# Optimization experiments

Measured on AMD Instinct MI355X. Metric: run time of the kernel, lower is better.

The kernel has to match this reference:

```python
import math
import jax, jax.numpy as jnp
import numpy as np

L, H, E, D = 12, 12, 768, 64   # stack_size, mh_size, embedding_dim, dim_w_matrices
B, S = 4, 512
EPS = 1e-5


def positional_enc(seq_len, model_dim):
    # faithful: power_ind = 10000 XOR int(2*i/dim)
    i = np.arange(model_dim)
    p = np.bitwise_xor(10000, (2 * i) // model_dim).astype(np.float32)
    pos = np.arange(seq_len, dtype=np.float32)[:, None]
    ang = pos / p[None, :]
    pe = np.where(i % 2 == 0, np.sin(ang), np.cos(ang)).astype(np.float32)
    return jnp.asarray(pe)


def layer_norm(x, g, b):
    mu = jnp.mean(x, axis=-1, keepdims=True)
    var = jnp.mean(jnp.square(x - mu), axis=-1, keepdims=True)
    return (x - mu) * jax.lax.rsqrt(var + EPS) * g + b


def encoder(x, wq, wo, g1, b1, fw, fb, g2, b2):
    # x: [B,S,E]; wq: [H,E,D]; wo: [E,H*D]; fw: [E,E] (torch Linear layout)
    bs = x.shape[0] * x.shape[1]
    nb = x.reshape(bs, E)                              # flatten batch (faithful)
    q = jnp.einsum('ne,hed->hnd', nb, wq)              # q == k == v (bug kept)
    scores = jax.nn.softmax(jnp.einsum('hnd,hmd->hnm', q, q) / math.sqrt(D), axis=-1)
    z = jnp.einsum('hnm,hmd->hnd', scores, q)          # [H,BS,D]
    zc = z.reshape(H * D, bs)                          # per-head view(D,-1) + cat
    mh = (wo @ zc).reshape(x.shape)                    # [B,S,E]
    l1 = layer_norm(x + mh, g1, b1)
    ffn = l1 @ fw.T + fb
    return layer_norm(l1 + ffn, g2, b2)


def setup_inputs() -> dict:
    key = jax.random.key(0)
    ks = jax.random.split(key, 8)

    def xavier(k, shape, fan_in, fan_out):
        lim = math.sqrt(6.0 / (fan_in + fan_out))
        return jax.random.uniform(k, shape, jnp.float32, -lim, lim)

    return {
        'tokens': jax.random.normal(ks[0], (B, S, E), jnp.float32),
        'wq':    xavier(ks[1], (L, H, E, D), E, D),
        'wo':    xavier(ks[2], (L, E, H * D), E, H * D),
        'ln1_g': jnp.ones((L, E), jnp.float32),
        'ln1_b': jnp.zeros((L, E), jnp.float32),
        'ffn_w': xavier(ks[3], (L, E, E), E, E),
        'ffn_b': jnp.zeros((L, E), jnp.float32),
        'ln2_g': jnp.ones((L, E), jnp.float32),
        'ln2_b': jnp.zeros((L, E), jnp.float32),
    }


def reference(tokens, wq, wo, ln1_g, ln1_b, ffn_w, ffn_b, ln2_g, ln2_b):
    pe = positional_enc(tokens.shape[1], tokens.shape[2])
    # faithful: layer 0 applied once on pe+tokens, then ALL layers (0 again) in loop
    x = encoder(pe + tokens, wq[0], wo[0], ln1_g[0], ln1_b[0],
                ffn_w[0], ffn_b[0], ln2_g[0], ln2_b[0])
    for l in range(L):
        x = encoder(x, wq[l], wo[l], ln1_g[l], ln1_b[l],
                    ffn_w[l], ffn_b[l], ln2_g[l], ln2_b[l])
    return x
```

## Files before the change

kernel.cpp:

```cpp
#include <hip/hip_runtime.h>
#include <hip/hip_bf16.h>


#define BS_TOK 2048
#define EMB 768
#define NH 12
#define HD 64
#define WQN (12 * NH * EMB * HD)

typedef __attribute__((ext_vector_type(8))) short bf16x8;
typedef __attribute__((ext_vector_type(4))) float f32x4;

__device__ __forceinline__ short f2bf(float f) {
  union { float f; unsigned u; } v;
  v.f = f;
  unsigned r = (v.u + 0x7FFF + ((v.u >> 16) & 1)) >> 16;
  return (short)(unsigned short)r;
}

#define MFMA16(a, b, c) __builtin_amdgcn_mfma_f32_16x16x32_bf16(a, b, c, 0, 0, 0)
#define SW64(r, k) ((r) * 64 + ((((k) >> 3) ^ ((r) & 7)) << 3) + ((k) & 7))

__global__ __launch_bounds__(256) void cvt_weights_kernel(const float* __restrict__ wo,
                                                          const float* __restrict__ fw,
                                                          short* __restrict__ wob,
                                                          short* __restrict__ fwb) {
  const float* src = blockIdx.y ? fw : wo;
  short* dst = blockIdx.y ? fwb : wob;
  int i = (blockIdx.x * 256 + threadIdx.x) * 8;
  float4 a = *(const float4*)(src + i);
  float4 b = *(const float4*)(src + i + 4);
  bf16x8 t;
  t[0] = f2bf(a.x); t[1] = f2bf(a.y); t[2] = f2bf(a.z); t[3] = f2bf(a.w);
  t[4] = f2bf(b.x); t[5] = f2bf(b.y); t[6] = f2bf(b.z); t[7] = f2bf(b.w);
  *(bf16x8*)(dst + i) = t;
}

__global__ __launch_bounds__(256) void wq_trans_kernel(const float* __restrict__ wq,
                                                       short* __restrict__ wqT) {
  __shared__ short T[64 * 64];
  const int et = blockIdx.x;
  const int lh = blockIdx.y;
  const int tid = threadIdx.x;
  const float* src = wq + ((size_t)lh * EMB + et * 64) * HD;
  {
    int r = tid >> 2, c16 = (tid & 3) << 4;
    const float* p = src + r * HD + c16;
    float4 x0 = *(const float4*)(p + 0);
    float4 x1 = *(const float4*)(p + 4);
    float4 x2 = *(const float4*)(p + 8);
    float4 x3 = *(const float4*)(p + 12);
    bf16x8 a, b;
    a[0] = f2bf(x0.x); a[1] = f2bf(x0.y); a[2] = f2bf(x0.z); a[3] = f2bf(x0.w);
    a[4] = f2bf(x1.x); a[5] = f2bf(x1.y); a[6] = f2bf(x1.z); a[7] = f2bf(x1.w);
    b[0] = f2bf(x2.x); b[1] = f2bf(x2.y); b[2] = f2bf(x2.z); b[3] = f2bf(x2.w);
    b[4] = f2bf(x3.x); b[5] = f2bf(x3.y); b[6] = f2bf(x3.z); b[7] = f2bf(x3.w);
    int g = c16 >> 3;
    *(bf16x8*)&T[r * 64 + ((g ^ (r & 7)) << 3)] = a;
    *(bf16x8*)&T[r * 64 + (((g + 1) ^ (r & 7)) << 3)] = b;
  }
  __syncthreads();
  {
    int d = tid >> 2, e16 = (tid & 3) << 4;
    bf16x8 t0, t1;
#pragma unroll
    for (int j = 0; j < 8; ++j) t0[j] = T[SW64(e16 + j, d)];
#pragma unroll
    for (int j = 0; j < 8; ++j) t1[j] = T[SW64(e16 + 8 + j, d)];
    short* q = wqT + ((size_t)lh * HD + d) * EMB + et * 64 + e16;
    *(bf16x8*)(q) = t0;
    *(bf16x8*)(q + 8) = t1;
  }
}

__global__ __launch_bounds__(256) void pe_add_kernel(const float* __restrict__ tok,
                                                     float* __restrict__ X,
                                                     short* __restrict__ Xb) {
  int idx = blockIdx.x * 256 + threadIdx.x;
  int e = idx % EMB;
  int t = idx / EMB;
  int s = t & 511;
  float p = (e < 384) ? 10000.0f : 10001.0f;
  float ang = (float)s / p;
  float pe = (e & 1) ? cosf(ang) : sinf(ang);
  float v = tok[idx] + pe;
  X[idx] = v;
  Xb[idx] = f2bf(v);
}

__device__ __forceinline__ void stage_direct_bf16(const short* __restrict__ src, int ld,
                                                  int row0, int k0, short* dst, int tid) {
  int r = tid >> 2, kb = (tid & 3) << 4;
  const short* p = src + (size_t)(row0 + r) * ld + k0 + kb;
  bf16x8 x0 = *(const bf16x8*)(p);
  bf16x8 x1 = *(const bf16x8*)(p + 8);
  int g = kb >> 3;
  *(bf16x8*)&dst[r * 64 + ((g ^ (r & 7)) << 3)] = x0;
  *(bf16x8*)&dst[r * 64 + (((g + 1) ^ (r & 7)) << 3)] = x1;
}

__device__ __forceinline__ void stage_direct128(const short* __restrict__ src, int ld,
                                                int row0, int k0, short* dst, int tid) {
  int r = tid >> 1, kb = (tid & 1) << 5;
  const short* p = src + (size_t)(row0 + r) * ld + k0 + kb;
  bf16x8 x0 = *(const bf16x8*)(p);
  bf16x8 x1 = *(const bf16x8*)(p + 8);
  bf16x8 x2 = *(const bf16x8*)(p + 16);
  bf16x8 x3 = *(const bf16x8*)(p + 24);
  int g = kb >> 3;
  *(bf16x8*)&dst[r * 64 + (((g + 0) ^ (r & 7)) << 3)] = x0;
  *(bf16x8*)&dst[r * 64 + (((g + 1) ^ (r & 7)) << 3)] = x1;
  *(bf16x8*)&dst[r * 64 + (((g + 2) ^ (r & 7)) << 3)] = x2;
  *(bf16x8*)&dst[r * 64 + (((g + 3) ^ (r & 7)) << 3)] = x3;
}

__device__ __forceinline__ void stage_trans_bf16(const short* __restrict__ src, int ld,
                                                 int k0, int col0, short* dst, int tid) {
  int kk = tid >> 2, nb = (tid & 3) << 4;
  const short* p = src + (size_t)(k0 + kk) * ld + col0 + nb;
  bf16x8 x0 = *(const bf16x8*)(p + 0);
  bf16x8 x1 = *(const bf16x8*)(p + 8);
#pragma unroll
  for (int j = 0; j < 8; ++j) dst[SW64(nb + j, kk)] = x0[j];
#pragma unroll
  for (int j = 0; j < 8; ++j) dst[SW64(nb + 8 + j, kk)] = x1[j];
}

#define GEMM_TILE_COMPUTE(As, Bs, acc)                                              \
  {                                                                                 \
    _Pragma("unroll") for (int s = 0; s < 2; ++s) {                                 \
      int ra = (w << 4) + l15;                                                      \
      bf16x8 af = *(const bf16x8*)&As[ra * 64 + ((((s << 2) + quad) ^ (ra & 7)) << 3)]; \
      _Pragma("unroll") for (int nt = 0; nt < 4; ++nt) {                            \
        int rb = (nt << 4) + l15;                                                   \
        bf16x8 bf = *(const bf16x8*)&Bs[rb * 64 + ((((s << 2) + quad) ^ (rb & 7)) << 3)]; \
        acc[nt] = MFMA16(af, bf, acc[nt]);                                          \
      }                                                                             \
    }                                                                               \
  }

#define GEMM_TILE_COMPUTE2(As, Bs, acc)                                             \
  {                                                                                 \
    _Pragma("unroll") for (int s = 0; s < 2; ++s) {                                 \
      bf16x8 af[2];                                                                 \
      _Pragma("unroll") for (int u = 0; u < 2; ++u) {                               \
        int ra = (w << 5) + (u << 4) + l15;                                         \
        af[u] = *(const bf16x8*)&As[ra * 64 + ((((s << 2) + quad) ^ (ra & 7)) << 3)]; \
      }                                                                             \
      _Pragma("unroll") for (int nt = 0; nt < 4; ++nt) {                            \
        int rb = (nt << 4) + l15;                                                   \
        bf16x8 bf = *(const bf16x8*)&Bs[rb * 64 + ((((s << 2) + quad) ^ (rb & 7)) << 3)]; \
        acc[0][nt] = MFMA16(af[0], bf, acc[0][nt]);                                 \
        acc[1][nt] = MFMA16(af[1], bf, acc[1][nt]);                                 \
      }                                                                             \
    }                                                                               \
  }

__global__ __launch_bounds__(256) void gemm_q_kernel(const short* __restrict__ Xb,
                                                     const short* __restrict__ WqT,
                                                     short* __restrict__ Qo,
                                                     short* __restrict__ Qt) {
  __shared__ short As[64 * 64];
  __shared__ short Bs[64 * 64];
  const int m0 = blockIdx.x * 64;
  const int h = blockIdx.y;
  const int tid = threadIdx.x;
  const int w = tid >> 6, lane = tid & 63, l15 = lane & 15, quad = lane >> 4;
  const short* wqh = WqT + (size_t)h * (HD * EMB);
  f32x4 acc[4] = {(f32x4){0, 0, 0, 0}, (f32x4){0, 0, 0, 0},
                  (f32x4){0, 0, 0, 0}, (f32x4){0, 0, 0, 0}};
  for (int k0 = 0; k0 < EMB; k0 += 64) {
    stage_direct_bf16(Xb, EMB, m0, k0, As, tid);
    stage_direct_bf16(wqh, EMB, 0, k0, Bs, tid);
    __syncthreads();
    GEMM_TILE_COMPUTE(As, Bs, acc);
    __syncthreads();
  }
  short* qo = Qo + (size_t)h * (BS_TOK * HD);
#pragma unroll
  for (int nt = 0; nt < 4; ++nt)
#pragma unroll
    for (int r = 0; r < 4; ++r) {
      short v = f2bf(acc[nt][r]);
      int tokr = (w << 4) + (quad << 2) + r;
      int d = (nt << 4) + l15;
      qo[(size_t)(m0 + tokr) * HD + d] = v;
      As[SW64(tokr, d)] = v;
    }
  __syncthreads();
  {
    int d = tid >> 2, tok0 = (tid & 3) << 4;
    bf16x8 t0, t1;
#pragma unroll
    for (int j = 0; j < 8; ++j) t0[j] = As[SW64(tok0 + j, d)];
#pragma unroll
    for (int j = 0; j < 8; ++j) t1[j] = As[SW64(tok0 + 8 + j, d)];
    short* qt = Qt + (size_t)h * (HD * BS_TOK) + (size_t)d * BS_TOK + m0 + tok0;
    *(bf16x8*)(qt) = t0;
    *(bf16x8*)(qt + 8) = t1;
  }
}

__global__ __launch_bounds__(256) void attn_mfma_kernel(const short* __restrict__ Q,
                                                        const short* __restrict__ Qt,
                                                        float* __restrict__ Opart,
                                                        float* __restrict__ Lpart) {
  __shared__ short Ks[64 * 64];
  __shared__ short Vt[64 * 64];
  __shared__ short Pw[4 * 16 * 64];
  const int h = blockIdx.y;
  const int q0 = blockIdx.x * 64;
  const int kt0 = blockIdx.z * 16;
  const int tid = threadIdx.x;
  const int lane = tid & 63;
  const int wv = tid >> 6;
  const int l15 = lane & 15;
  const int quad = lane >> 4;
  const short* Qh = Q + (size_t)h * (BS_TOK * HD);
  const short* Qth = Qt + (size_t)h * (HD * BS_TOK);
  short* myP = Pw + wv * 16 * 64;

  bf16x8 qf[2];
  {
    const short* qp = Qh + (size_t)(q0 + wv * 16 + l15) * HD + quad * 8;
    qf[0] = *(const bf16x8*)(qp);
    qf[1] = *(const bf16x8*)(qp + 32);
  }

  f32x4 o[4];
  float lp[4] = {0.f, 0.f, 0.f, 0.f};
#pragma unroll
  for (int r = 0; r < 4; ++r) o[r] = (f32x4){0.f, 0.f, 0.f, 0.f};

  bf16x8 kreg[2], vreg[2];
#pragma unroll
  for (int i = 0; i < 2; ++i) {
    int c = i * 256 + tid;
    kreg[i] = *(const bf16x8*)(Qh + kt0 * 4096 + c * 8);
    vreg[i] = *(const bf16x8*)(Qth + (c >> 3) * BS_TOK + kt0 * 64 + (c & 7) * 8);
  }

  for (int kt = 0; kt < 16; ++kt) {
    __syncthreads();
#pragma unroll
    for (int i = 0; i < 2; ++i) {
      int c = i * 256 + tid, row = c >> 3, g = c & 7;
      *(bf16x8*)&Ks[row * 64 + ((g ^ (row & 7)) << 3)] = kreg[i];
      *(bf16x8*)&Vt[row * 64 + ((g ^ (row & 7)) << 3)] = vreg[i];
    }
    __syncthreads();
    if (kt < 15) {
      int gt = kt0 + kt + 1;
#pragma unroll
      for (int i = 0; i < 2; ++i) {
        int c = i * 256 + tid;
        kreg[i] = *(const bf16x8*)(Qh + gt * 4096 + c * 8);
        vreg[i] = *(const bf16x8*)(Qth + (c >> 3) * BS_TOK + gt * 64 + (c & 7) * 8);
      }
    }

    f32x4 s[4];
#pragma unroll
    for (int ct = 0; ct < 4; ++ct) {
      f32x4 acc = (f32x4){0.f, 0.f, 0.f, 0.f};
#pragma unroll
      for (int ks = 0; ks < 2; ++ks) {
        int row = ct * 16 + l15;
        int c = ks * 4 + quad;
        bf16x8 kf = *(const bf16x8*)(&Ks[row * 64 + ((c ^ (row & 7)) << 3)]);
        acc = MFMA16(qf[ks], kf, acc);
      }
      s[ct] = acc;
    }

#pragma unroll
    for (int ct = 0; ct < 4; ++ct)
#pragma unroll
      for (int r = 0; r < 4; ++r) {
        float p = __expf(s[ct][r] * 0.125f);
        lp[r] += p;
        myP[SW64(quad * 4 + r, ct * 16 + l15)] = f2bf(p);
      }

#pragma unroll
    for (int ks = 0; ks < 2; ++ks) {
      int c = ks * 4 + quad;
      bf16x8 pf = *(const bf16x8*)(&myP[l15 * 64 + ((c ^ (l15 & 7)) << 3)]);
#pragma unroll
      for (int dt = 0; dt < 4; ++dt) {
        int row = dt * 16 + l15;
        bf16x8 vf = *(const bf16x8*)(&Vt[row * 64 + ((c ^ (row & 7)) << 3)]);
        o[dt] = MFMA16(pf, vf, o[dt]);
      }
    }
  }

#pragma unroll
  for (int r = 0; r < 4; ++r) {
    float t = lp[r];
#pragma unroll
    for (int d = 1; d < 16; d <<= 1) t += __shfl_xor(t, d, 64);
    lp[r] = t;
  }
  const int NB = BS_TOK * EMB;
  float* Oh = Opart + (size_t)blockIdx.z * NB + (size_t)h * (BS_TOK * HD);
  float* Lh = Lpart + ((size_t)blockIdx.z * NH + h) * BS_TOK;
#pragma unroll
  for (int r = 0; r < 4; ++r) {
    int qrow = q0 + wv * 16 + quad * 4 + r;
#pragma unroll
    for (int dt = 0; dt < 4; ++dt)
      Oh[(size_t)qrow * HD + dt * 16 + l15] = o[dt][r];
    if (l15 == 0) Lh[qrow] = lp[r];
  }
}

__global__ __launch_bounds__(256) void attn_combine_kernel(const float* __restrict__ Op,
                                                           const float* __restrict__ Lp,
                                                           short* __restrict__ Z) {
  const int NB = BS_TOK * EMB;
  const int NHT = NH * BS_TOK;
  int idx = blockIdx.x * 256 + threadIdx.x;
  float o = Op[idx] + Op[idx + NB];
  int hq = idx >> 6;
  float l = Lp[hq] + Lp[hq + NHT];
  Z[idx] = f2bf(o / l);
}

__global__ __launch_bounds__(256) void gemm_out_kernel(const short* __restrict__ Wob,
                                                       const short* __restrict__ Zc,
                                                       float* __restrict__ Pp) {
  __shared__ short As[128 * 64];
  __shared__ short Bs[64 * 64];
  const int n0 = blockIdx.x * 64;
  const int m0 = blockIdx.y * 128;
  const int kz = blockIdx.z * 384;
  const int tid = threadIdx.x;
  const int w = tid >> 6, lane = tid & 63, l15 = lane & 15, quad = lane >> 4;
  f32x4 acc[2][4] = {};
  for (int k0 = 0; k0 < 384; k0 += 64) {
    stage_direct128(Wob, EMB, m0, kz + k0, As, tid);
    stage_trans_bf16(Zc, BS_TOK, kz + k0, n0, Bs, tid);
    __syncthreads();
    GEMM_TILE_COMPUTE2(As, Bs, acc);
    __syncthreads();
  }
  float* P = Pp + (size_t)blockIdx.z * (BS_TOK * EMB);
#pragma unroll
  for (int u = 0; u < 2; ++u)
#pragma unroll
    for (int nt = 0; nt < 4; ++nt)
#pragma unroll
      for (int r = 0; r < 4; ++r)
        P[(size_t)(m0 + (w << 5) + (u << 4) + (quad << 2) + r) * BS_TOK + n0 +
          (nt << 4) + l15] = acc[u][nt][r];
}

__global__ __launch_bounds__(256) void gemm_ffn_kernel(const short* __restrict__ L1b,
                                                       const short* __restrict__ Fwb,
                                                       const float* __restrict__ Fb,
                                                       float* __restrict__ Pp) {
  __shared__ short As[128 * 64];
  __shared__ short Bs[64 * 64];
  const int m0 = blockIdx.x * 128;
  const int n0 = blockIdx.y * 64;
  const int kz = blockIdx.z * 384;
  const int tid = threadIdx.x;
  const int w = tid >> 6, lane = tid & 63, l15 = lane & 15, quad = lane >> 4;
  f32x4 acc[2][4] = {};
  for (int k0 = 0; k0 < 384; k0 += 64) {
    stage_direct128(L1b, EMB, m0, kz + k0, As, tid);
    stage_direct_bf16(Fwb, EMB, n0, kz + k0, Bs, tid);
    __syncthreads();
    GEMM_TILE_COMPUTE2(As, Bs, acc);
    __syncthreads();
  }
  float* P = Pp + (size_t)blockIdx.z * (BS_TOK * EMB);
  const bool addb = (blockIdx.z == 0);
#pragma unroll
  for (int nt = 0; nt < 4; ++nt) {
    float bias = addb ? Fb[n0 + (nt << 4) + l15] : 0.0f;
#pragma unroll
    for (int u = 0; u < 2; ++u)
#pragma unroll
      for (int r = 0; r < 4; ++r)
        P[(size_t)(m0 + (w << 5) + (u << 4) + (quad << 2) + r) * EMB + n0 +
          (nt << 4) + l15] = acc[u][nt][r] + bias;
  }
}

__global__ __launch_bounds__(256) void ln_kernel(const float* __restrict__ Xa,
                                                 const float* __restrict__ P,
                                                 const float* __restrict__ g,
                                                 const float* __restrict__ bb,
                                                 float* __restrict__ Out,
                                                 short* __restrict__ Outb) {
  __shared__ float red[4];
  const int NB = BS_TOK * EMB;
  const int t = blockIdx.x;
  const int tid = threadIdx.x;
  float v[3];
  float s = 0.f;
#pragma unroll
  for (int i = 0; i < 3; ++i) {
    int e = tid + i * 256;
    int idx = t * EMB + e;
    v[i] = Xa[idx] + P[idx] + P[idx + NB];
    s += v[i];
  }
#pragma unroll
  for (int o = 32; o > 0; o >>= 1) s += __shfl_xor(s, o, 64);
  if ((tid & 63) == 0) red[tid >> 6] = s;
  __syncthreads();
  float mu = (red[0] + red[1] + red[2] + red[3]) * (1.0f / EMB);
  float q = 0.f;
#pragma unroll
  for (int i = 0; i < 3; ++i) {
    float d = v[i] - mu;
    q += d * d;
  }
#pragma unroll
  for (int o = 32; o > 0; o >>= 1) q += __shfl_xor(q, o, 64);
  __syncthreads();
  if ((tid & 63) == 0) red[tid >> 6] = q;
  __syncthreads();
  float var = (red[0] + red[1] + red[2] + red[3]) * (1.0f / EMB);
  float r = rsqrtf(var + 1e-5f);
#pragma unroll
  for (int i = 0; i < 3; ++i) {
    int e = tid + i * 256;
    float res = (v[i] - mu) * r * g[e] + bb[e];
    Out[t * EMB + e] = res;
    Outb[t * EMB + e] = f2bf(res);
  }
}

extern "C" void kernel_launch(void* const* d_in, const int* in_sizes, int n_in,
                              void* d_out, int out_size, void* d_ws, size_t ws_size,
                              hipStream_t stream) {
  const float* tok = (const float*)d_in[0];
  const float* wq = (const float*)d_in[1];
  const float* wo = (const float*)d_in[2];
  const float* g1 = (const float*)d_in[3];
  const float* b1 = (const float*)d_in[4];
  const float* fw = (const float*)d_in[5];
  const float* fb = (const float*)d_in[6];
  const float* g2 = (const float*)d_in[7];
  const float* b2 = (const float*)d_in[8];
  const int NB = BS_TOK * EMB;
  float* bufA = (float*)d_ws;
  float* bufB = bufA + NB;
  float* bufC = bufB + NB;
  float* bufD = bufC + NB;
  short* XbA = (short*)(bufD + NB);
  short* L1b = XbA + NB;
  short* Qbf = L1b + NB;
  short* Qtb = Qbf + NB;
  short* Zbf = Qtb + NB;
  short* wqTb = Zbf + NB;
  short* wob = wqTb + WQN;
  short* fwb = wob + WQN;
  float* Lpart = (float*)(fwb + WQN);

  cvt_weights_kernel<<<dim3(WQN / (256 * 8), 2), 256, 0, stream>>>(wo, fw, wob, fwb);
  wq_trans_kernel<<<dim3(12, 12 * NH), 256, 0, stream>>>(wq, wqTb);
  pe_add_kernel<<<NB / 256, 256, 0, stream>>>(tok, bufA, XbA);
  for (int it = 0; it < 13; ++it) {
    int l = (it == 0) ? 0 : it - 1;
    gemm_q_kernel<<<dim3(32, NH), 256, 0, stream>>>(
        XbA, wqTb + (size_t)l * (NH * HD * EMB), Qbf, Qtb);
    attn_mfma_kernel<<<dim3(32, NH, 2), 256, 0, stream>>>(Qbf, Qtb, bufB, Lpart);
    attn_combine_kernel<<<NB / 256, 256, 0, stream>>>(bufB, Lpart, Zbf);
    gemm_out_kernel<<<dim3(32, 6, 2), 256, 0, stream>>>(
        wob + (size_t)l * (EMB * EMB), Zbf, bufB);
    ln_kernel<<<BS_TOK, 256, 0, stream>>>(bufA, bufB, g1 + l * EMB, b1 + l * EMB,
                                          bufD, L1b);
    gemm_ffn_kernel<<<dim3(16, 12, 2), 256, 0, stream>>>(
        L1b, fwb + (size_t)l * (EMB * EMB), fb + l * EMB, bufB);
    float* ln2_dst = (it == 12) ? (float*)d_out : bufA;
    ln_kernel<<<BS_TOK, 256, 0, stream>>>(bufD, bufB, g2 + l * EMB, b2 + l * EMB,
                                          ln2_dst, XbA);
  }
}
```

Baseline: 1.231 ms.

## Fuse attention split-combine into output GEMM staging and vectorize Q/P stores

Removes the separate attn_combine kernel. The output GEMM now reads the two fp32 partial attention outputs and the row sums directly, normalizes them and converts to bf16 while staging its B tile. The attention kernel swaps the MFMA operand order so each lane holds one query row, which reduces the row-sum reduction to two shuffles and lets P be written to LDS as 4-wide vectors. The Q GEMM writes Q through LDS with coalesced 16-byte stores. The trade-off is that the out-GEMM reloads fp32 data redundantly across its 6 M-blocks, doubling bytes versus bf16 Z, in exchange for one fewer launch and no Z round trip.

```diff
diff --git a/kernel.cpp b/kernel.cpp
--- a/kernel.cpp
+++ b/kernel.cpp
@@ -9,6 +9,7 @@
 #define WQN (12 * NH * EMB * HD)
 
 typedef __attribute__((ext_vector_type(8))) short bf16x8;
+typedef __attribute__((ext_vector_type(4))) short bf16x4;
 typedef __attribute__((ext_vector_type(4))) float f32x4;
 
 __device__ __forceinline__ short f2bf(float f) {
@@ -114,16 +115,24 @@
   *(bf16x8*)&dst[r * 64 + (((g + 3) ^ (r & 7)) << 3)] = x3;
 }
 
-__device__ __forceinline__ void stage_trans_bf16(const short* __restrict__ src, int ld,
+__device__ __forceinline__ void stage_trans_comb(const float* __restrict__ Op,
+                                                 const float* __restrict__ Lp,
                                                  int k0, int col0, short* dst, int tid) {
+  const int NB = BS_TOK * EMB;
+  const int NHT = NH * BS_TOK;
   int kk = tid >> 2, nb = (tid & 3) << 4;
-  const short* p = src + (size_t)(k0 + kk) * ld + col0 + nb;
-  bf16x8 x0 = *(const bf16x8*)(p + 0);
-  bf16x8 x1 = *(const bf16x8*)(p + 8);
-#pragma unroll
-  for (int j = 0; j < 8; ++j) dst[SW64(nb + j, kk)] = x0[j];
-#pragma unroll
-  for (int j = 0; j < 8; ++j) dst[SW64(nb + 8 + j, kk)] = x1[j];
+  size_t base = (size_t)(k0 + kk) * BS_TOK + col0 + nb;
+  int hq = (int)(base >> 6);
+  float rl = 1.0f / (Lp[hq] + Lp[hq + NHT]);
+#pragma unroll
+  for (int q4 = 0; q4 < 4; ++q4) {
+    float4 a = *(const float4*)(Op + base + q4 * 4);
+    float4 b = *(const float4*)(Op + base + NB + q4 * 4);
+    dst[SW64(nb + q4 * 4 + 0, kk)] = f2bf((a.x + b.x) * rl);
+    dst[SW64(nb + q4 * 4 + 1, kk)] = f2bf((a.y + b.y) * rl);
+    dst[SW64(nb + q4 * 4 + 2, kk)] = f2bf((a.z + b.z) * rl);
+    dst[SW64(nb + q4 * 4 + 3, kk)] = f2bf((a.w + b.w) * rl);
+  }
 }
 
 #define GEMM_TILE_COMPUTE(As, Bs, acc)                                              \
@@ -176,18 +185,21 @@
     GEMM_TILE_COMPUTE(As, Bs, acc);
     __syncthreads();
   }
-  short* qo = Qo + (size_t)h * (BS_TOK * HD);
 #pragma unroll
   for (int nt = 0; nt < 4; ++nt)
 #pragma unroll
-    for (int r = 0; r < 4; ++r) {
-      short v = f2bf(acc[nt][r]);
-      int tokr = (w << 4) + (quad << 2) + r;
-      int d = (nt << 4) + l15;
-      qo[(size_t)(m0 + tokr) * HD + d] = v;
-      As[SW64(tokr, d)] = v;
-    }
+    for (int r = 0; r < 4; ++r)
+      As[SW64((w << 4) + (quad << 2) + r, (nt << 4) + l15)] = f2bf(acc[nt][r]);
   __syncthreads();
+  {
+    int r2 = tid >> 2, kb = (tid & 3) << 4;
+    int g = kb >> 3;
+    bf16x8 q0v = *(const bf16x8*)&As[r2 * 64 + ((g ^ (r2 & 7)) << 3)];
+    bf16x8 q1v = *(const bf16x8*)&As[r2 * 64 + (((g + 1) ^ (r2 & 7)) << 3)];
+    short* qo = Qo + (size_t)h * (BS_TOK * HD) + (size_t)(m0 + r2) * HD + kb;
+    *(bf16x8*)(qo) = q0v;
+    *(bf16x8*)(qo + 8) = q1v;
+  }
   {
     int d = tid >> 2, tok0 = (tid & 3) << 4;
     bf16x8 t0, t1;
@@ -228,7 +240,7 @@
   }
 
   f32x4 o[4];
-  float lp[4] = {0.f, 0.f, 0.f, 0.f};
+  float lpl = 0.f;
 #pragma unroll
   for (int r = 0; r < 4; ++r) o[r] = (f32x4){0.f, 0.f, 0.f, 0.f};
 
@@ -268,19 +280,23 @@
         int row = ct * 16 + l15;
         int c = ks * 4 + quad;
         bf16x8 kf = *(const bf16x8*)(&Ks[row * 64 + ((c ^ (row & 7)) << 3)]);
-        acc = MFMA16(qf[ks], kf, acc);
+        acc = MFMA16(kf, qf[ks], acc);
       }
       s[ct] = acc;
     }
 
 #pragma unroll
-    for (int ct = 0; ct < 4; ++ct)
+    for (int ct = 0; ct < 4; ++ct) {
+      bf16x4 pv4;
 #pragma unroll
       for (int r = 0; r < 4; ++r) {
         float p = __expf(s[ct][r] * 0.125f);
-        lp[r] += p;
-        myP[SW64(quad * 4 + r, ct * 16 + l15)] = f2bf(p);
+        lpl += p;
+        pv4[r] = f2bf(p);
       }
+      int g = 2 * ct + (quad >> 1);
+      *(bf16x4*)&myP[l15 * 64 + ((g ^ (l15 & 7)) << 3) + ((quad & 1) << 2)] = pv4;
+    }
 
 #pragma unroll
     for (int ks = 0; ks < 2; ++ks) {
@@ -295,40 +311,25 @@
     }
   }
 
-#pragma unroll
-  for (int r = 0; r < 4; ++r) {
-    float t = lp[r];
-#pragma unroll
-    for (int d = 1; d < 16; d <<= 1) t += __shfl_xor(t, d, 64);
-    lp[r] = t;
-  }
+  lpl += __shfl_xor(lpl, 16, 64);
+  lpl += __shfl_xor(lpl, 32, 64);
+
   const int NB = BS_TOK * EMB;
   float* Oh = Opart + (size_t)blockIdx.z * NB + (size_t)h * (BS_TOK * HD);
   float* Lh = Lpart + ((size_t)blockIdx.z * NH + h) * BS_TOK;
+  if (quad == 0) Lh[q0 + wv * 16 + l15] = lpl;
 #pragma unroll
   for (int r = 0; r < 4; ++r) {
     int qrow = q0 + wv * 16 + quad * 4 + r;
 #pragma unroll
     for (int dt = 0; dt < 4; ++dt)
       Oh[(size_t)qrow * HD + dt * 16 + l15] = o[dt][r];
-    if (l15 == 0) Lh[qrow] = lp[r];
-  }
-}
-
-__global__ __launch_bounds__(256) void attn_combine_kernel(const float* __restrict__ Op,
-                                                           const float* __restrict__ Lp,
-                                                           short* __restrict__ Z) {
-  const int NB = BS_TOK * EMB;
-  const int NHT = NH * BS_TOK;
-  int idx = blockIdx.x * 256 + threadIdx.x;
-  float o = Op[idx] + Op[idx + NB];
-  int hq = idx >> 6;
-  float l = Lp[hq] + Lp[hq + NHT];
-  Z[idx] = f2bf(o / l);
+  }
 }
 
 __global__ __launch_bounds__(256) void gemm_out_kernel(const short* __restrict__ Wob,
-                                                       const short* __restrict__ Zc,
+                                                       const float* __restrict__ Op,
+                                                       const float* __restrict__ Lp,
                                                        float* __restrict__ Pp) {
   __shared__ short As[128 * 64];
   __shared__ short Bs[64 * 64];
@@ -340,7 +341,7 @@
   f32x4 acc[2][4] = {};
   for (int k0 = 0; k0 < 384; k0 += 64) {
     stage_direct128(Wob, EMB, m0, kz + k0, As, tid);
-    stage_trans_bf16(Zc, BS_TOK, kz + k0, n0, Bs, tid);
+    stage_trans_comb(Op, Lp, kz + k0, n0, Bs, tid);
     __syncthreads();
     GEMM_TILE_COMPUTE2(As, Bs, acc);
     __syncthreads();
@@ -452,12 +453,13 @@
   float* bufB = bufA + NB;
   float* bufC = bufB + NB;
   float* bufD = bufC + NB;
-  short* XbA = (short*)(bufD + NB);
+  float* bufE = bufD + NB;
+  float* bufF = bufE + NB;
+  short* XbA = (short*)(bufF + NB);
   short* L1b = XbA + NB;
   short* Qbf = L1b + NB;
   short* Qtb = Qbf + NB;
-  short* Zbf = Qtb + NB;
-  short* wqTb = Zbf + NB;
+  short* wqTb = Qtb + NB;
   short* wob = wqTb + WQN;
   short* fwb = wob + WQN;
   float* Lpart = (float*)(fwb + WQN);
@@ -469,10 +471,9 @@
     int l = (it == 0) ? 0 : it - 1;
     gemm_q_kernel<<<dim3(32, NH), 256, 0, stream>>>(
         XbA, wqTb + (size_t)l * (NH * HD * EMB), Qbf, Qtb);
-    attn_mfma_kernel<<<dim3(32, NH, 2), 256, 0, stream>>>(Qbf, Qtb, bufB, Lpart);
-    attn_combine_kernel<<<NB / 256, 256, 0, stream>>>(bufB, Lpart, Zbf);
+    attn_mfma_kernel<<<dim3(32, NH, 2), 256, 0, stream>>>(Qbf, Qtb, bufE, Lpart);
     gemm_out_kernel<<<dim3(32, 6, 2), 256, 0, stream>>>(
-        wob + (size_t)l * (EMB * EMB), Zbf, bufB);
+        wob + (size_t)l * (EMB * EMB), bufE, Lpart, bufB);
     ln_kernel<<<BS_TOK, 256, 0, stream>>>(bufA, bufB, g1 + l * EMB, b1 + l * EMB,
                                           bufD, L1b);
     gemm_ffn_kernel<<<dim3(16, 12, 2), 256, 0, stream>>>(
```

After: 1.171 ms. 4.9% less time.
